# Optimization experiments

Hardware: AMD Instinct MI355X
Metric: run time of the kernel (lower is better)

The kernel has to match this reference:

```python
import jax, jax.numpy as jnp
import numpy as np

H = 64   # hidden size
T = 28   # timesteps (rows)
V = 28   # features per step (cols)
L = 7    # rnn layers
SCALE = 1.0 / np.sqrt(H)  # torch nn.RNN init bound


def setup_inputs() -> dict:
    key = jax.random.key(0)
    ks = jax.random.split(key, 8)
    N = 65536
    return {
        "x":    jax.random.normal(ks[0], (N, T, V), jnp.float32),
        "Wih0": jax.random.normal(ks[1], (H, V), jnp.float32) * SCALE,
        "Wih":  jax.random.normal(ks[2], (L - 1, H, H), jnp.float32) * SCALE,
        "Whh":  jax.random.normal(ks[3], (L, H, H), jnp.float32) * SCALE,
        "bih":  jax.random.normal(ks[4], (L, H), jnp.float32) * SCALE,
        "bhh":  jax.random.normal(ks[5], (L, H), jnp.float32) * SCALE,
        "Wc":   jax.random.normal(ks[6], (10, H), jnp.float32) * SCALE,
        "bc":   jax.random.normal(ks[7], (10,), jnp.float32) * SCALE,
    }


def _rnn_layer(x_seq, wih, whh, bi, bh):
    # x_seq: (N, T, in). Precompute input projection for all timesteps (one big GEMM),
    # then scan the recurrence over time.
    xp = jnp.einsum("nti,hi->nth", x_seq, wih) + bi  # (N, T, H)
    h0 = jnp.zeros((x_seq.shape[0], whh.shape[0]), x_seq.dtype)

    def step(h, xt):  # xt: (N, H)
        h_new = jnp.tanh(xt + h @ whh.T + bh)
        return h_new, h_new

    _, hs = jax.lax.scan(step, h0, jnp.swapaxes(xp, 0, 1))  # hs: (T, N, H)
    return jnp.swapaxes(hs, 0, 1)  # (N, T, H)


def reference(x, Wih0, Wih, Whh, bih, bhh, Wc, bc):
    seq = x.reshape(-1, T, V)
    h = _rnn_layer(seq, Wih0, Whh[0], bih[0], bhh[0])
    for l in range(1, L):
        h = _rnn_layer(h, Wih[l - 1], Whh[l], bih[l], bhh[l])
    last = h[:, -1, :]               # (N, H) — last timestep of top layer
    return last @ Wc.T + bc          # (N, 10)
```

## Files before the change

kernel.cpp:

```cpp
#include <hip/hip_runtime.h>


namespace {

typedef __attribute__((ext_vector_type(8))) short bf16x8;
typedef __attribute__((ext_vector_type(4))) float f32x4;
typedef __attribute__((ext_vector_type(4))) unsigned u32x4;

constexpr int WST = 0;
constexpr int SCR = 7 * 16384;
constexpr int WCL = SCR + 8 * 2048;
constexpr int BIA = WCL + 2048;
constexpr int BCV = BIA + 1792;
constexpr int LDS_TOTAL = BCV + 64;

constexpr float TANH_K = 2.8853900817779268f;

__device__ __forceinline__ float tanh_pre(float a) {
    float z = __builtin_amdgcn_exp2f(a);
    return fmaf(-2.f, __builtin_amdgcn_rcpf(z + 1.f), 1.f);
}
__device__ __forceinline__ unsigned cvt_pk(float a, float b) {
    unsigned r;
    asm("v_cvt_pk_bf16_f32 %0, %1, %2" : "=v"(r) : "v"(a), "v"(b));
    return r;
}
__device__ __forceinline__ int4 pack8s(const float* v, float s) {
    return make_int4((int)cvt_pk(v[0] * s, v[1] * s), (int)cvt_pk(v[2] * s, v[3] * s),
                     (int)cvt_pk(v[4] * s, v[5] * s), (int)cvt_pk(v[6] * s, v[7] * s));
}
__device__ __forceinline__ bf16x8 pk8(float4 a, float4 b) {
    u32x4 t;
    t[0] = cvt_pk(a.x, a.y); t[1] = cvt_pk(a.z, a.w);
    t[2] = cvt_pk(b.x, b.y); t[3] = cvt_pk(b.z, b.w);
    return __builtin_bit_cast(bf16x8, t);
}

}

__global__ void __launch_bounds__(512, 1)
rnn_fused(const float* __restrict__ x,    const float* __restrict__ Wih0,
          const float* __restrict__ Wih,  const float* __restrict__ Whh,
          const float* __restrict__ bih,  const float* __restrict__ bhh,
          const float* __restrict__ Wc,   const float* __restrict__ bc,
          float* __restrict__ out)
{
    extern __shared__ char smem[];
    const int tid  = threadIdx.x;
    const int lane = tid & 63;
    const int wid  = tid >> 6;
    const int sl   = lane & 15;
    const int g    = lane >> 4;
    const int swzS = (sl & 7) << 4;
    const int seqbase = blockIdx.x * 128 + wid * 16;

    const int rd0 = (g * 16) ^ swzS;
    const int rd1 = (64 + g * 16) ^ swzS;
    int wro[4];
#pragma unroll
    for (int jt = 0; jt < 4; ++jt) wro[jt] = (jt * 32 + g * 8) ^ swzS;
    const int scrw = SCR + wid * 2048 + sl * 128;

    {
        const int j = tid >> 3, k0 = (tid & 7) * 8;
        const int wz = (k0 * 2) ^ ((j & 7) << 4);
#pragma unroll
        for (int l = 0; l < 7; ++l) {
            float v[8];
            if (l == 0) {
#pragma unroll
                for (int e = 0; e < 8; ++e)
                    v[e] = (k0 + e < 28) ? Wih0[j * 28 + k0 + e] : 0.f;
            } else {
                const float* src = Wih + (size_t)(l - 1) * 4096 + j * 64 + k0;
                float4 a4 = *(const float4*)(src);
                float4 b4 = *(const float4*)(src + 4);
                v[0]=a4.x; v[1]=a4.y; v[2]=a4.z; v[3]=a4.w;
                v[4]=b4.x; v[5]=b4.y; v[6]=b4.z; v[7]=b4.w;
            }
            *(int4*)(smem + WST + l * 16384 + j * 128 + wz) = pack8s(v, TANH_K);
            const float* srh = Whh + (size_t)l * 4096 + j * 64 + k0;
            float4 a4 = *(const float4*)(srh);
            float4 b4 = *(const float4*)(srh + 4);
            float w[8] = {a4.x, a4.y, a4.z, a4.w, b4.x, b4.y, b4.z, b4.w};
            *(int4*)(smem + WST + l * 16384 + 8192 + j * 128 + wz) = pack8s(w, TANH_K);
        }
    }
    if (tid < 128) {
        int c = tid >> 3, k0 = (tid & 7) * 8;
        float v[8];
#pragma unroll
        for (int e = 0; e < 8; ++e) v[e] = (c < 10) ? Wc[c * 64 + k0 + e] : 0.f;
        *(int4*)(smem + WCL + c * 128 + ((k0 * 2) ^ ((c & 7) << 4))) = pack8s(v, 1.f);
    }
    if (tid < 448) *(float*)(smem + BIA + tid * 4) = (bih[tid] + bhh[tid]) * TANH_K;
    if (tid < 16)  *(float*)(smem + BCV + tid * 4) = (tid < 10) ? bc[tid] : 0.f;
    __syncthreads();

    const bf16x8 zf = {};
    bf16x8 hb0[7], hb1[7];
#pragma unroll
    for (int l = 0; l < 7; ++l) { hb0[l] = zf; hb1[l] = zf; }

    const float* xr = x + (size_t)(seqbase + sl) * 784 + g * 8;
    const float4 z4 = make_float4(0.f, 0.f, 0.f, 0.f);

#pragma unroll 1
    for (int tq = 0; tq < 7; ++tq) {
        const float* p0 = xr + tq * 112;
        bf16x8 xf[4];
#pragma unroll
        for (int s = 0; s < 4; ++s) {
            float4 a0 = *(const float4*)(p0 + s * 28);
            float4 a1 = (g < 3) ? *(const float4*)(p0 + s * 28 + 4) : z4;
            xf[s] = pk8(a0, a1);
        }

        bf16x8 itA[4], itB[4];

#pragma unroll
        for (int l = 0; l < 7; ++l) {
            const int wb = WST + l * 16384;
            bf16x8 wi0[4], wi1[4], wh0[4], wh1[4];
            f32x4  bs[4];
#pragma unroll
            for (int jt = 0; jt < 4; ++jt) {
                const int ro = wb + (jt * 16 + sl) * 128;
                wi0[jt] = *(const bf16x8*)(smem + ro + rd0);
                if (l) wi1[jt] = *(const bf16x8*)(smem + ro + rd1);
                wh0[jt] = *(const bf16x8*)(smem + ro + 8192 + rd0);
                wh1[jt] = *(const bf16x8*)(smem + ro + 8192 + rd1);
                bs[jt]  = *(const f32x4*)(smem + BIA + l * 256 + jt * 64 + g * 16);
            }
            bf16x8 hp0 = hb0[l], hp1 = hb1[l];

#pragma unroll
            for (int s = 0; s < 4; ++s) {
                const bf16x8 i0 = l ? itA[s] : xf[s];
                const bf16x8 i1 = l ? itB[s] : zf;
#pragma unroll
                for (int jt = 0; jt < 4; ++jt) {
                    f32x4 a = bs[jt];
                    a = __builtin_amdgcn_mfma_f32_16x16x32_bf16(wi0[jt], i0, a, 0, 0, 0);
                    if (l) a = __builtin_amdgcn_mfma_f32_16x16x32_bf16(wi1[jt], i1, a, 0, 0, 0);
                    a = __builtin_amdgcn_mfma_f32_16x16x32_bf16(wh0[jt], hp0, a, 0, 0, 0);
                    a = __builtin_amdgcn_mfma_f32_16x16x32_bf16(wh1[jt], hp1, a, 0, 0, 0);
                    unsigned q0 = cvt_pk(tanh_pre(a[0]), tanh_pre(a[1]));
                    unsigned q1 = cvt_pk(tanh_pre(a[2]), tanh_pre(a[3]));
                    *(int2*)(smem + scrw + wro[jt]) = make_int2((int)q0, (int)q1);
                }
                hp0 = *(const bf16x8*)(smem + scrw + rd0);
                hp1 = *(const bf16x8*)(smem + scrw + rd1);
                itA[s] = hp0;
                itB[s] = hp1;
            }
            hb0[l] = hp0; hb1[l] = hp1;
        }
    }

    {
        const int ro = WCL + sl * 128;
        bf16x8 w0 = *(const bf16x8*)(smem + ro + rd0);
        bf16x8 w1 = *(const bf16x8*)(smem + ro + rd1);
        f32x4 o = {0.f, 0.f, 0.f, 0.f};
        o = __builtin_amdgcn_mfma_f32_16x16x32_bf16(w0, hb0[6], o, 0, 0, 0);
        o = __builtin_amdgcn_mfma_f32_16x16x32_bf16(w1, hb1[6], o, 0, 0, 0);
        f32x4 bb = *(const f32x4*)(smem + BCV + g * 16);
#pragma unroll
        for (int r = 0; r < 4; ++r) {
            const int c = g * 4 + r;
            if (c < 10)
                out[(size_t)(seqbase + sl) * 10 + c] = o[r] + bb[r];
        }
    }
}

extern "C" void kernel_launch(void* const* d_in, const int* in_sizes, int n_in,
                              void* d_out, int out_size, void* d_ws, size_t ws_size,
                              hipStream_t stream) {
    (void)in_sizes; (void)n_in; (void)d_ws; (void)ws_size; (void)out_size;
    hipFuncSetAttribute((const void*)rnn_fused,
                        hipFuncAttributeMaxDynamicSharedMemorySize, LDS_TOTAL);
    rnn_fused<<<dim3(512), dim3(512), LDS_TOTAL, stream>>>(
        (const float*)d_in[0], (const float*)d_in[1], (const float*)d_in[2],
        (const float*)d_in[3], (const float*)d_in[4], (const float*)d_in[5],
        (const float*)d_in[6], (const float*)d_in[7], (float*)d_out);
}
```

Measured before the change: 267.6 us.

## Stream layer weights through a 3-layer LDS bank to cut shared memory

Instead of staging all seven layers' bf16 weights in LDS once at kernel start (~135 KB), the kernel now reloads weights from global memory in groups of up to three layers per time chunk. The groups go into a 48 KB LDS bank, which brings total LDS down to about 69 KB so two 512-thread blocks could fit per CU. The cost is reconverting and rewriting weights 21 times per block, plus extra block-wide barriers inside the time loop that stall all waves. Launch bounds still say one block per SM, so whether occupancy actually rises is uncertain.

```diff
diff --git a/kernel.cpp b/kernel.cpp
--- a/kernel.cpp
+++ b/kernel.cpp
@@ -7,12 +7,12 @@
 typedef __attribute__((ext_vector_type(4))) float f32x4;
 typedef __attribute__((ext_vector_type(4))) unsigned u32x4;
 
-constexpr int WST = 0;
-constexpr int SCR = 7 * 16384;
-constexpr int WCL = SCR + 8 * 2048;
-constexpr int BIA = WCL + 2048;
-constexpr int BCV = BIA + 1792;
-constexpr int LDS_TOTAL = BCV + 64;
+constexpr int WBANK = 0;
+constexpr int SCR   = 49152;
+constexpr int WCL   = 65536;
+constexpr int BIA   = 67584;
+constexpr int BCV   = 69376;
+constexpr int LDS_TOTAL = 69440;
 
 constexpr float TANH_K = 2.8853900817779268f;
 
@@ -61,31 +61,9 @@
     for (int jt = 0; jt < 4; ++jt) wro[jt] = (jt * 32 + g * 8) ^ swzS;
     const int scrw = SCR + wid * 2048 + sl * 128;
 
-    {
-        const int j = tid >> 3, k0 = (tid & 7) * 8;
-        const int wz = (k0 * 2) ^ ((j & 7) << 4);
-#pragma unroll
-        for (int l = 0; l < 7; ++l) {
-            float v[8];
-            if (l == 0) {
-#pragma unroll
-                for (int e = 0; e < 8; ++e)
-                    v[e] = (k0 + e < 28) ? Wih0[j * 28 + k0 + e] : 0.f;
-            } else {
-                const float* src = Wih + (size_t)(l - 1) * 4096 + j * 64 + k0;
-                float4 a4 = *(const float4*)(src);
-                float4 b4 = *(const float4*)(src + 4);
-                v[0]=a4.x; v[1]=a4.y; v[2]=a4.z; v[3]=a4.w;
-                v[4]=b4.x; v[5]=b4.y; v[6]=b4.z; v[7]=b4.w;
-            }
-            *(int4*)(smem + WST + l * 16384 + j * 128 + wz) = pack8s(v, TANH_K);
-            const float* srh = Whh + (size_t)l * 4096 + j * 64 + k0;
-            float4 a4 = *(const float4*)(srh);
-            float4 b4 = *(const float4*)(srh + 4);
-            float w[8] = {a4.x, a4.y, a4.z, a4.w, b4.x, b4.y, b4.z, b4.w};
-            *(int4*)(smem + WST + l * 16384 + 8192 + j * 128 + wz) = pack8s(w, TANH_K);
-        }
-    }
+    const int js  = tid >> 3, k0s = (tid & 7) * 8;
+    const int wzs = (k0s * 2) ^ ((js & 7) << 4);
+
     if (tid < 128) {
         int c = tid >> 3, k0 = (tid & 7) * 8;
         float v[8];
@@ -95,7 +73,6 @@
     }
     if (tid < 448) *(float*)(smem + BIA + tid * 4) = (bih[tid] + bhh[tid]) * TANH_K;
     if (tid < 16)  *(float*)(smem + BCV + tid * 4) = (tid < 10) ? bc[tid] : 0.f;
-    __syncthreads();
 
     const bf16x8 zf = {};
     bf16x8 hb0[7], hb1[7];
@@ -119,42 +96,74 @@
         bf16x8 itA[4], itB[4];
 
 #pragma unroll
-        for (int l = 0; l < 7; ++l) {
-            const int wb = WST + l * 16384;
-            bf16x8 wi0[4], wi1[4], wh0[4], wh1[4];
-            f32x4  bs[4];
+        for (int b = 0; b < 3; ++b) {
+            const int L0 = 3 * b;
+            const int NB = (b == 2) ? 1 : 3;
+
+            __syncthreads();
 #pragma unroll
-            for (int jt = 0; jt < 4; ++jt) {
-                const int ro = wb + (jt * 16 + sl) * 128;
-                wi0[jt] = *(const bf16x8*)(smem + ro + rd0);
-                if (l) wi1[jt] = *(const bf16x8*)(smem + ro + rd1);
-                wh0[jt] = *(const bf16x8*)(smem + ro + 8192 + rd0);
-                wh1[jt] = *(const bf16x8*)(smem + ro + 8192 + rd1);
-                bs[jt]  = *(const f32x4*)(smem + BIA + l * 256 + jt * 64 + g * 16);
+            for (int dl = 0; dl < NB; ++dl) {
+                const int l = L0 + dl;
+                float v[8];
+                if (l == 0) {
+#pragma unroll
+                    for (int e = 0; e < 8; ++e)
+                        v[e] = (k0s + e < 28) ? Wih0[js * 28 + k0s + e] : 0.f;
+                } else {
+                    const float* src = Wih + (size_t)(l - 1) * 4096 + js * 64 + k0s;
+                    float4 a4 = *(const float4*)(src);
+                    float4 b4 = *(const float4*)(src + 4);
+                    v[0]=a4.x; v[1]=a4.y; v[2]=a4.z; v[3]=a4.w;
+                    v[4]=b4.x; v[5]=b4.y; v[6]=b4.z; v[7]=b4.w;
+                }
+                *(int4*)(smem + WBANK + dl * 16384 + js * 128 + wzs) = pack8s(v, TANH_K);
+                const float* srh = Whh + (size_t)l * 4096 + js * 64 + k0s;
+                float4 a4 = *(const float4*)(srh);
+                float4 b4 = *(const float4*)(srh + 4);
+                float w[8] = {a4.x, a4.y, a4.z, a4.w, b4.x, b4.y, b4.z, b4.w};
+                *(int4*)(smem + WBANK + dl * 16384 + 8192 + js * 128 + wzs) = pack8s(w, TANH_K);
             }
-            bf16x8 hp0 = hb0[l], hp1 = hb1[l];
+            __syncthreads();
 
 #pragma unroll
-            for (int s = 0; s < 4; ++s) {
-                const bf16x8 i0 = l ? itA[s] : xf[s];
-                const bf16x8 i1 = l ? itB[s] : zf;
+            for (int dl = 0; dl < NB; ++dl) {
+                const int l  = L0 + dl;
+                const int wb = WBANK + dl * 16384;
+                bf16x8 wi0[4], wi1[4], wh0[4], wh1[4];
+                f32x4  bs[4];
 #pragma unroll
                 for (int jt = 0; jt < 4; ++jt) {
-                    f32x4 a = bs[jt];
-                    a = __builtin_amdgcn_mfma_f32_16x16x32_bf16(wi0[jt], i0, a, 0, 0, 0);
-                    if (l) a = __builtin_amdgcn_mfma_f32_16x16x32_bf16(wi1[jt], i1, a, 0, 0, 0);
-                    a = __builtin_amdgcn_mfma_f32_16x16x32_bf16(wh0[jt], hp0, a, 0, 0, 0);
-                    a = __builtin_amdgcn_mfma_f32_16x16x32_bf16(wh1[jt], hp1, a, 0, 0, 0);
-                    unsigned q0 = cvt_pk(tanh_pre(a[0]), tanh_pre(a[1]));
-                    unsigned q1 = cvt_pk(tanh_pre(a[2]), tanh_pre(a[3]));
-                    *(int2*)(smem + scrw + wro[jt]) = make_int2((int)q0, (int)q1);
+                    const int ro = wb + (jt * 16 + sl) * 128;
+                    wi0[jt] = *(const bf16x8*)(smem + ro + rd0);
+                    if (l) wi1[jt] = *(const bf16x8*)(smem + ro + rd1);
+                    wh0[jt] = *(const bf16x8*)(smem + ro + 8192 + rd0);
+                    wh1[jt] = *(const bf16x8*)(smem + ro + 8192 + rd1);
+                    bs[jt]  = *(const f32x4*)(smem + BIA + l * 256 + jt * 64 + g * 16);
                 }
-                hp0 = *(const bf16x8*)(smem + scrw + rd0);
-                hp1 = *(const bf16x8*)(smem + scrw + rd1);
-                itA[s] = hp0;
-                itB[s] = hp1;
+                bf16x8 hp0 = hb0[l], hp1 = hb1[l];
+
+#pragma unroll
+                for (int s = 0; s < 4; ++s) {
+                    const bf16x8 i0 = l ? itA[s] : xf[s];
+                    const bf16x8 i1 = l ? itB[s] : zf;
+#pragma unroll
+                    for (int jt = 0; jt < 4; ++jt) {
+                        f32x4 a = bs[jt];
+                        a = __builtin_amdgcn_mfma_f32_16x16x32_bf16(wi0[jt], i0, a, 0, 0, 0);
+                        if (l) a = __builtin_amdgcn_mfma_f32_16x16x32_bf16(wi1[jt], i1, a, 0, 0, 0);
+                        a = __builtin_amdgcn_mfma_f32_16x16x32_bf16(wh0[jt], hp0, a, 0, 0, 0);
+                        a = __builtin_amdgcn_mfma_f32_16x16x32_bf16(wh1[jt], hp1, a, 0, 0, 0);
+                        unsigned q0 = cvt_pk(tanh_pre(a[0]), tanh_pre(a[1]));
+                        unsigned q1 = cvt_pk(tanh_pre(a[2]), tanh_pre(a[3]));
+                        *(int2*)(smem + scrw + wro[jt]) = make_int2((int)q0, (int)q1);
+                    }
+                    hp0 = *(const bf16x8*)(smem + scrw + rd0);
+                    hp1 = *(const bf16x8*)(smem + scrw + rd1);
+                    itA[s] = hp0;
+                    itB[s] = hp1;
+                }
+                hb0[l] = hp0; hb1[l] = hp1;
             }
-            hb0[l] = hp0; hb1[l] = hp1;
         }
     }
 
```

Result: slower. 321.7 us (+20.2%).
